# Performance work log

Hardware: AMD Instinct MI355X
Metric: run time of the kernel (lower is better)

The kernel has to match this reference:

```python
import jax, jax.numpy as jnp
import numpy as np
from jax.scipy.linalg import solve_triangular

B, S, HIDDEN = 2, 2048, 2048
HK, HV, DK, DV = 16, 32, 128, 128
KCONV = 4
CHUNK = 64
EPS = 1e-6
KEY_DIM = HK * DK        # 2048
VALUE_DIM = HV * DV      # 4096
CONV_DIM = 2 * KEY_DIM + VALUE_DIM  # 8192


def setup_inputs() -> dict:
    key = jax.random.key(0)
    ks = jax.random.split(key, 8)
    s = lambda n: 1.0 / np.sqrt(n)
    return {
        "hidden_states": jax.random.normal(ks[0], (B, S, HIDDEN), jnp.float32),
        "W_qkvz": jax.random.normal(ks[1], (HIDDEN, 2 * KEY_DIM + 2 * VALUE_DIM), jnp.float32) * s(HIDDEN),
        "W_ba": jax.random.normal(ks[2], (HIDDEN, 2 * HV), jnp.float32) * s(HIDDEN),
        "conv_weight": jax.random.normal(ks[3], (CONV_DIM, KCONV), jnp.float32) * s(KCONV),
        "dt_bias": jnp.ones((HV,), jnp.float32),
        "A_log": jax.random.normal(ks[4], (HV,), jnp.float32) * 0.1,
        "norm_weight": jnp.ones((DV,), jnp.float32),
        "W_out": jax.random.normal(ks[5], (VALUE_DIM, HIDDEN), jnp.float32) * s(VALUE_DIM),
    }


def _chunk_gated_delta_rule(q, k, v, g, beta):
    # q,k: [B,H,S,DK] (l2-normalized); v: [B,H,S,DV]; g,beta: [B,H,S]
    Bq, H, Sq, Dk = q.shape
    N = Sq // CHUNK
    q = q * (Dk ** -0.5)
    rs = lambda x: x.reshape(Bq, H, N, CHUNK, x.shape[-1])
    q, k, v = rs(q), rs(k), rs(v)
    g = g.reshape(Bq, H, N, CHUNK)
    beta = beta.reshape(Bq, H, N, CHUNK)
    gc = jnp.cumsum(g, axis=-1)  # within-chunk cumulative log-decay
    tri = jnp.tril(jnp.ones((CHUNK, CHUNK), bool))
    tri_s = jnp.tril(jnp.ones((CHUNK, CHUNK), bool), -1)
    decay = jnp.where(tri, jnp.exp(gc[..., :, None] - gc[..., None, :]), 0.0)
    k_beta = k * beta[..., None]
    v_beta = v * beta[..., None]
    # strictly-lower within-chunk interaction matrix; T = (I + A)^{-1} (fwd substitution)
    A = jnp.where(tri_s, jnp.einsum('bhncd,bhnkd->bhnck', k_beta, k) * decay, 0.0)
    eye = jnp.eye(CHUNK, dtype=q.dtype)
    T = solve_triangular(eye + A, jnp.broadcast_to(eye, A.shape), lower=True)
    v_adj = T @ v_beta                                    # [B,H,N,C,DV]
    k_cumdecay = T @ (k_beta * jnp.exp(gc)[..., None])    # [B,H,N,C,DK]
    attn_local = jnp.where(tri, jnp.einsum('bhncd,bhnkd->bhnck', q, k) * decay, 0.0)

    def step(state, xs):
        q_i, k_i, vadj_i, kcd_i, g_i, attn_i = xs          # per-chunk slices [B,H,C,*]
        v_new = vadj_i - kcd_i @ state                     # [B,H,C,DV]
        o = (q_i * jnp.exp(g_i)[..., None]) @ state + attn_i @ v_new
        g_last = g_i[..., -1]                              # [B,H]
        decayed_k = k_i * jnp.exp(g_last[..., None] - g_i)[..., None]
        state = state * jnp.exp(g_last)[..., None, None] + jnp.einsum('bhcd,bhcv->bhdv', decayed_k, v_new)
        return state, o

    mv = lambda x: jnp.moveaxis(x, 2, 0)
    state0 = jnp.zeros((Bq, H, Dk, v.shape[-1]), q.dtype)
    _, o = jax.lax.scan(step, state0, (mv(q), mv(k), mv(v_adj), mv(k_cumdecay), mv(gc), mv(attn_local)))
    return jnp.moveaxis(o, 0, 2).reshape(Bq, H, Sq, -1)


def reference(hidden_states, W_qkvz, W_ba, conv_weight, dt_bias, A_log, norm_weight, W_out):
    B_, S_, _ = hidden_states.shape
    # fused QKVZ / BA projections, contiguous layout [q|k|v|z], [b|a]
    qkvz = hidden_states @ W_qkvz
    q, k, v, z = jnp.split(qkvz, [KEY_DIM, 2 * KEY_DIM, 2 * KEY_DIM + VALUE_DIM], axis=-1)
    b, a = jnp.split(hidden_states @ W_ba, 2, axis=-1)
    beta = jax.nn.sigmoid(b)                                   # [B,S,HV]
    g = -jnp.exp(A_log) * jax.nn.softplus(a + dt_bias)         # [B,S,HV]
    # causal depthwise conv over [q|k|v] channels + silu
    mixed = jnp.concatenate([q, k, v], axis=-1)                # [B,S,CONV_DIM]
    pad = jnp.pad(mixed, ((0, 0), (KCONV - 1, 0), (0, 0)))
    conv = sum(pad[:, j:j + S_, :] * conv_weight[:, j] for j in range(KCONV))
    conv = jax.nn.silu(conv)
    q, k, v = jnp.split(conv, [KEY_DIM, 2 * KEY_DIM], axis=-1)
    q = q.reshape(B_, S_, HK, DK)
    k = k.reshape(B_, S_, HK, DK)
    v = v.reshape(B_, S_, HV, DV)
    l2n = lambda x: x * jax.lax.rsqrt(jnp.sum(x * x, -1, keepdims=True) + 1e-6)
    q, k = l2n(q), l2n(k)
    rep = HV // HK  # each qk head serves rep consecutive v heads
    q = jnp.repeat(q, rep, axis=2)
    k = jnp.repeat(k, rep, axis=2)
    tr = lambda x: jnp.swapaxes(x, 1, 2)                       # -> [B,H,S,D]
    o = _chunk_gated_delta_rule(tr(q), tr(k), tr(v), jnp.swapaxes(g, 1, 2), jnp.swapaxes(beta, 1, 2))
    o = jnp.swapaxes(o, 1, 2)                                  # [B,S,HV,DV]
    # gated RMSNorm (norm before gate): rmsnorm(o) * w * silu(z)
    z = z.reshape(B_, S_, HV, DV)
    o = o * jax.lax.rsqrt(jnp.mean(o * o, -1, keepdims=True) + EPS)
    o = o * norm_weight * jax.nn.silu(z)
    return o.reshape(B_, S_, VALUE_DIM) @ W_out
```

## Files before the change

### kernel.cpp

```cpp
#include <hip/hip_runtime.h>
#include <hip/hip_bf16.h>


typedef short bf16x8 __attribute__((ext_vector_type(8)));
typedef float f32x4  __attribute__((ext_vector_type(4)));

#define MFMA_BF16(a,b,c) __builtin_amdgcn_mfma_f32_16x16x32_bf16((a),(b),(c),0,0,0)
#define GLD16(g,l) __builtin_amdgcn_global_load_lds((const __attribute__((address_space(1))) void*)(g), (__attribute__((address_space(3))) void*)(l), 16, 0, 0)

__device__ __forceinline__ unsigned short f2bf(float x){
  union { float f; unsigned u; } v; v.f = x;
  return (unsigned short)((v.u + 0x7fffu + ((v.u >> 16) & 1u)) >> 16);
}
__device__ __forceinline__ float bf2f(unsigned short h){
  union { unsigned u; float f; } v; v.u = ((unsigned)h) << 16; return v.f;
}
__device__ __forceinline__ unsigned long long pack4bf(float a, float b, float c, float d){
  return (unsigned long long)f2bf(a) | ((unsigned long long)f2bf(b) << 16)
       | ((unsigned long long)f2bf(c) << 32) | ((unsigned long long)f2bf(d) << 48);
}

__global__ __launch_bounds__(256) void cast_bf16_kernel(
    const float* __restrict__ in, unsigned short* __restrict__ out, int n)
{
  int i = (blockIdx.x * 256 + threadIdx.x) * 4;
  if (i >= n) return;
  float4 v = *(const float4*)(in + i);
  *(unsigned long long*)(out + i) = pack4bf(v.x, v.y, v.z, v.w);
}

__global__ __launch_bounds__(256) void transpose_cast_kernel(
    const float* __restrict__ W, unsigned short* __restrict__ WT, int R, int C)
{
  __shared__ __attribute__((aligned(16))) float tile[32][33];
  int c0 = blockIdx.x * 32, r0 = blockIdx.y * 32;
  int tx = threadIdx.x & 31, ty = threadIdx.x >> 5;
  #pragma unroll
  for (int i = 0; i < 32; i += 8)
    tile[ty + i][tx] = W[(size_t)(r0 + ty + i) * C + c0 + tx];
  __syncthreads();
  #pragma unroll
  for (int i = 0; i < 32; i += 8)
    WT[(size_t)(c0 + ty + i) * R + r0 + tx] = f2bf(tile[tx][ty + i]);
}

__global__ __launch_bounds__(512, 2) void gemm256_bt(
    const unsigned short* __restrict__ A,
    const unsigned short* __restrict__ B,
    unsigned short* __restrict__ C, int M, int N, int K)
{
  __shared__ __attribute__((aligned(16))) unsigned short lds[65536];

  const int tid  = threadIdx.x;
  const int wave = tid >> 6, lane = tid & 63;
  const int quad = lane >> 4, l16 = lane & 15;
  const int wm8 = (wave >> 2) << 3;
  const int wn4 = (wave & 3) << 2;

  int wg = blockIdx.x;
  if ((gridDim.x & 7) == 0) {
    int qq = (int)gridDim.x >> 3;
    wg = (wg & 7) * qq + (wg >> 3);
  }
  const int tm = M >> 8;
  const int m0 = (wg % tm) << 8;
  const int n0 = (wg / tm) << 8;

  const int rd_off = ((l16 << 6) + (quad << 4)) ^ ((l16 >> 3) << 5);

  const int st_off = wave << 9;
  const int src_c  = ((wave & 1) << 5) + (((lane & 3) << 3) ^ ((lane >> 5) << 4));
  const unsigned short* Asrc = A + (size_t)(m0 + ((wave >> 1) << 4) + (lane >> 2)) * K + src_c;
  const unsigned short* Bsrc = B + (size_t)(n0 + ((wave >> 1) << 4) + (lane >> 2)) * K + src_c;

  const int NT = K >> 6;

#define STA(t, qi) GLD16(Asrc + (size_t)(qi) * 64 * K + (t) * 64, \
                         lds + (((t) & 1) << 15) + st_off + ((qi) << 12))
#define STB(t, qi) GLD16(Bsrc + (size_t)(qi) * 64 * K + (t) * 64, \
                         lds + (((t) & 1) << 15) + 16384 + st_off + ((qi) << 12))
#define RDA(dst, P)                                                            \
  _Pragma("unroll")                                                            \
  for (int j = 0; j < 2; ++j)                                                  \
    _Pragma("unroll")                                                          \
    for (int kb = 0; kb < 2; ++kb)                                             \
      dst[j][kb] = *(const bf16x8*)(Ar + ((((wm8 + 2 * (P) + j) << 1) | kb) << 10) + rd_off);
#define MMA(P, AF)                                                             \
  __builtin_amdgcn_s_setprio(1);                                               \
  _Pragma("unroll")                                                            \
  for (int j = 0; j < 2; ++j)                                                  \
    _Pragma("unroll")                                                          \
    for (int nf = 0; nf < 4; ++nf)                                             \
      _Pragma("unroll")                                                        \
      for (int kb = 0; kb < 2; ++kb)                                           \
        acc[2 * (P) + j][nf] = MFMA_BF16(AF[j][kb], b8[nf][kb], acc[2 * (P) + j][nf]); \
  __builtin_amdgcn_s_setprio(0);
#define LGKM4  asm volatile("s_waitcnt lgkmcnt(4)" ::: "memory");              \
               __builtin_amdgcn_sched_barrier(0)
#define LGKM0  asm volatile("s_waitcnt lgkmcnt(0)" ::: "memory");              \
               __builtin_amdgcn_sched_barrier(0)

  f32x4 acc[8][4];
  #pragma unroll
  for (int a = 0; a < 8; ++a)
    #pragma unroll
    for (int b = 0; b < 4; ++b)
      #pragma unroll
      for (int r = 0; r < 4; ++r) acc[a][b][r] = 0.f;

  STB(0, 0); STB(0, 1); STB(0, 2); STB(0, 3);
  STA(0, 0); STA(0, 1); STA(0, 2); STA(0, 3);
  if (NT > 1) {
    STB(1, 0); STB(1, 1); STB(1, 2); STB(1, 3); STA(1, 0); STA(1, 2);
    asm volatile("s_waitcnt vmcnt(6)" ::: "memory");
  } else {
    asm volatile("s_waitcnt vmcnt(0)" ::: "memory");
  }
  __builtin_amdgcn_s_barrier();

  for (int u = 0; u < NT; ++u) {
    const char* Ar = (const char*)lds + ((u & 1) << 16);
    const char* Br = Ar + 32768;
    bf16x8 b8[4][2], aA[2][2], aB[2][2];
    #pragma unroll
    for (int nf = 0; nf < 4; ++nf)
      #pragma unroll
      for (int kb = 0; kb < 2; ++kb)
        b8[nf][kb] = *(const bf16x8*)(Br + ((((wn4 + nf) << 1) | kb) << 10) + rd_off);
    RDA(aA, 0);
    __builtin_amdgcn_sched_barrier(0);

    RDA(aB, 1);
    if (u + 1 < NT) { STA(u + 1, 1); STA(u + 1, 3); }
    __builtin_amdgcn_s_barrier();
    LGKM4;
    MMA(0, aA);
    __builtin_amdgcn_s_barrier();

    RDA(aA, 2);
    if (u + 2 < NT) { STB(u + 2, 0); STB(u + 2, 1); }
    __builtin_amdgcn_s_barrier();
    LGKM4;
    MMA(1, aB);
    __builtin_amdgcn_s_barrier();

    RDA(aB, 3);
    if (u + 2 < NT) { STB(u + 2, 2); STA(u + 2, 0); }
    __builtin_amdgcn_s_barrier();
    LGKM4;
    MMA(2, aA);
    __builtin_amdgcn_s_barrier();

    if (u + 2 < NT) { STB(u + 2, 3); STA(u + 2, 2); }
    __builtin_amdgcn_s_barrier();
    LGKM0;
    MMA(3, aB);
    if (u + 2 < NT) asm volatile("s_waitcnt vmcnt(6)" ::: "memory");
    else            asm volatile("s_waitcnt vmcnt(0)" ::: "memory");
    __builtin_amdgcn_s_barrier();
  }
#undef RDA
#undef MMA
#undef LGKM4
#undef LGKM0
#undef STA
#undef STB

  #pragma unroll
  for (int mt = 0; mt < 8; ++mt) {
    int row = m0 + ((wave >> 2) << 7) + mt * 16 + (quad << 2);
    #pragma unroll
    for (int nf = 0; nf < 4; ++nf) {
      int col = n0 + ((wave & 3) << 6) + nf * 16 + l16;
      #pragma unroll
      for (int r = 0; r < 4; ++r)
        C[(size_t)(row + r) * N + col] = f2bf(acc[mt][nf][r]);
    }
  }
}

__global__ __launch_bounds__(512, 2) void gemm128x256_bt(
    const unsigned short* __restrict__ A,
    const unsigned short* __restrict__ B,
    float* __restrict__ C, int M, int N, int K)
{
  __shared__ __attribute__((aligned(16))) unsigned short lds[49152];

  const int tid  = threadIdx.x;
  const int wave = tid >> 6, lane = tid & 63;
  const int quad = lane >> 4, l16 = lane & 15;
  const int wm4 = (wave >> 2) << 2;
  const int wn4 = (wave & 3) << 2;

  int wg = blockIdx.x;
  if ((gridDim.x & 7) == 0) {
    int qq = (int)gridDim.x >> 3;
    wg = (wg & 7) * qq + (wg >> 3);
  }
  const int tm = M >> 7;
  const int m0 = (wg % tm) << 7;
  const int n0 = (wg / tm) << 8;

  const int rd_off = ((l16 << 6) + (quad << 4)) ^ ((l16 >> 3) << 5);
  const int st_off = wave << 9;
  const int src_c  = ((wave & 1) << 5) + (((lane & 3) << 3) ^ ((lane >> 5) << 4));
  const unsigned short* Asrc = A + (size_t)(m0 + ((wave >> 1) << 4) + (lane >> 2)) * K + src_c;
  const unsigned short* Bsrc = B + (size_t)(n0 + ((wave >> 1) << 4) + (lane >> 2)) * K + src_c;

  const int NT = K >> 6;

#define STA(t, qi) GLD16(Asrc + (size_t)(qi) * 64 * K + (t) * 64, \
                         lds + (((t) & 1) * 24576) + st_off + ((qi) << 12))
#define STB(t, qi) GLD16(Bsrc + (size_t)(qi) * 64 * K + (t) * 64, \
                         lds + (((t) & 1) * 24576) + 8192 + st_off + ((qi) << 12))

  f32x4 acc[4][4];
  #pragma unroll
  for (int a = 0; a < 4; ++a)
    #pragma unroll
    for (int b = 0; b < 4; ++b)
      #pragma unroll
      for (int r = 0; r < 4; ++r) acc[a][b][r] = 0.f;

  STB(0, 0); STB(0, 1); STB(0, 2); STB(0, 3);
  STA(0, 0); STA(0, 1);
  if (NT > 1) {
    STB(1, 0); STB(1, 1); STB(1, 2); STB(1, 3);
    asm volatile("s_waitcnt vmcnt(4)" ::: "memory");
  } else {
    asm volatile("s_waitcnt vmcnt(0)" ::: "memory");
  }
  __builtin_amdgcn_s_barrier();

  for (int u = 0; u < NT; ++u) {
    const char* Ar = (const char*)lds + (u & 1) * 49152;
    const char* Br = Ar + 16384;
    bf16x8 b8[4][2], aA[2][2], aB[2][2];
    #pragma unroll
    for (int nf = 0; nf < 4; ++nf)
      #pragma unroll
      for (int kb = 0; kb < 2; ++kb)
        b8[nf][kb] = *(const bf16x8*)(Br + ((((wn4 + nf) << 1) | kb) << 10) + rd_off);
    #pragma unroll
    for (int j = 0; j < 2; ++j)
      #pragma unroll
      for (int kb = 0; kb < 2; ++kb)
        aA[j][kb] = *(const bf16x8*)(Ar + ((((wm4 + j) << 1) | kb) << 10) + rd_off);
    __builtin_amdgcn_sched_barrier(0);

    #pragma unroll
    for (int j = 0; j < 2; ++j)
      #pragma unroll
      for (int kb = 0; kb < 2; ++kb)
        aB[j][kb] = *(const bf16x8*)(Ar + ((((wm4 + 2 + j) << 1) | kb) << 10) + rd_off);
    if (u + 1 < NT) { STA(u + 1, 0); STA(u + 1, 1); }
    __builtin_amdgcn_s_barrier();
    asm volatile("s_waitcnt lgkmcnt(4)" ::: "memory");
    __builtin_amdgcn_sched_barrier(0);
    __builtin_amdgcn_s_setprio(1);
    #pragma unroll
    for (int j = 0; j < 2; ++j)
      #pragma unroll
      for (int nf = 0; nf < 4; ++nf)
        #pragma unroll
        for (int kb = 0; kb < 2; ++kb)
          acc[j][nf] = MFMA_BF16(aA[j][kb], b8[nf][kb], acc[j][nf]);
    __builtin_amdgcn_s_setprio(0);
    __builtin_amdgcn_s_barrier();

    if (u + 2 < NT) { STB(u + 2, 0); STB(u + 2, 1); STB(u + 2, 2); STB(u + 2, 3); }
    __builtin_amdgcn_s_barrier();
    asm volatile("s_waitcnt lgkmcnt(0)" ::: "memory");
    __builtin_amdgcn_sched_barrier(0);
    __builtin_amdgcn_s_setprio(1);
    #pragma unroll
    for (int j = 0; j < 2; ++j)
      #pragma unroll
      for (int nf = 0; nf < 4; ++nf)
        #pragma unroll
        for (int kb = 0; kb < 2; ++kb)
          acc[2 + j][nf] = MFMA_BF16(aB[j][kb], b8[nf][kb], acc[2 + j][nf]);
    __builtin_amdgcn_s_setprio(0);
    if (u + 2 < NT) asm volatile("s_waitcnt vmcnt(4)" ::: "memory");
    else            asm volatile("s_waitcnt vmcnt(0)" ::: "memory");
    __builtin_amdgcn_s_barrier();
  }
#undef STA
#undef STB

  #pragma unroll
  for (int mt = 0; mt < 4; ++mt) {
    int row = m0 + ((wave >> 2) << 6) + mt * 16 + (quad << 2);
    #pragma unroll
    for (int nf = 0; nf < 4; ++nf) {
      int col = n0 + ((wave & 3) << 6) + nf * 16 + l16;
      #pragma unroll
      for (int r = 0; r < 4; ++r)
        C[(size_t)(row + r) * N + col] = acc[mt][nf][r];
    }
  }
}

__global__ __launch_bounds__(256) void ba_kernel(
    const float* __restrict__ H, const float* __restrict__ Wba,
    const float* __restrict__ dtb, const float* __restrict__ Alog,
    float* __restrict__ bbuf, float* __restrict__ gbuf)
{
  int t = threadIdx.x;
  int col = t & 63, wv = t >> 6;
  int m0 = blockIdx.x * 16 + wv * 4;
  const float* h0 = H + (size_t)m0 * 2048;
  float a0 = 0.f, a1 = 0.f, a2 = 0.f, a3 = 0.f;
  for (int k = 0; k < 2048; ++k) {
    float w = Wba[k * 64 + col];
    a0 += h0[k]        * w;
    a1 += h0[2048 + k] * w;
    a2 += h0[4096 + k] * w;
    a3 += h0[6144 + k] * w;
  }
  float accv[4] = {a0, a1, a2, a3};
  #pragma unroll
  for (int r = 0; r < 4; ++r) {
    int m = m0 + r;
    int b = m >> 11, s = m & 2047;
    float acc = accv[r];
    if (col < 32) {
      bbuf[((size_t)(b * 32 + col)) * 2048 + s] = 1.f / (1.f + __expf(-acc));
    } else {
      int hh = col - 32;
      float x  = acc + dtb[hh];
      float sp = (x > 20.f) ? x : log1pf(__expf(x));
      gbuf[((size_t)(b * 32 + hh)) * 2048 + s] = -__expf(Alog[hh]) * sp;
    }
  }
}

__global__ __launch_bounds__(128) void conv_kernel(
    const unsigned short* __restrict__ qkvz, const float* __restrict__ cw,
    unsigned short* __restrict__ qn, unsigned short* __restrict__ kn,
    unsigned short* __restrict__ vb)
{
  int s_base = blockIdx.x * 4;
  int head   = blockIdx.y * 8 + (threadIdx.x >> 4);
  int c8     = (threadIdx.x & 15) * 8;
  int col    = head * 128 + c8;
  int s_loc  = s_base & 2047;

  float vin[7][8];
  #pragma unroll
  for (int t = 0; t < 7; ++t) {
    int sp = s_loc + t - 3;
    if (sp >= 0) {
      bf16x8 v = *(const bf16x8*)(qkvz + (size_t)(s_base + t - 3) * 12288 + col);
      #pragma unroll
      for (int j = 0; j < 8; ++j) vin[t][j] = bf2f((unsigned short)v[j]);
    } else {
      #pragma unroll
      for (int j = 0; j < 8; ++j) vin[t][j] = 0.f;
    }
  }
  float w[8][4];
  #pragma unroll
  for (int j = 0; j < 8; ++j) {
    float4 wv = *(const float4*)(cw + (size_t)(col + j) * 4);
    w[j][0] = wv.x; w[j][1] = wv.y; w[j][2] = wv.z; w[j][3] = wv.w;
  }
  float y[4][8];
  #pragma unroll
  for (int u = 0; u < 4; ++u)
    #pragma unroll
    for (int j = 0; j < 8; ++j) {
      float acc = vin[u][j]*w[j][0] + vin[u+1][j]*w[j][1]
                + vin[u+2][j]*w[j][2] + vin[u+3][j]*w[j][3];
      y[u][j] = acc / (1.f + __expf(-acc));
    }

  if (head < 32) {
    #pragma unroll
    for (int u = 0; u < 4; ++u) {
      float ss = 0.f;
      #pragma unroll
      for (int j = 0; j < 8; ++j) ss += y[u][j] * y[u][j];
      ss += __shfl_xor(ss, 1);
      ss += __shfl_xor(ss, 2);
      ss += __shfl_xor(ss, 4);
      ss += __shfl_xor(ss, 8);
      float r = rsqrtf(ss + 1e-6f);
      bf16x8 out;
      if (head < 16) {
        float rq = r * 0.08838834764831845f;
        #pragma unroll
        for (int j = 0; j < 8; ++j) out[j] = (short)f2bf(y[u][j] * rq);
        *(bf16x8*)(qn + ((size_t)(s_base + u) * 16 + head) * 128 + c8) = out;
      } else {
        #pragma unroll
        for (int j = 0; j < 8; ++j) out[j] = (short)f2bf(y[u][j] * r);
        *(bf16x8*)(kn + ((size_t)(s_base + u) * 16 + (head - 16)) * 128 + c8) = out;
      }
    }
  } else {
    #pragma unroll
    for (int u = 0; u < 4; ++u) {
      bf16x8 out;
      #pragma unroll
      for (int j = 0; j < 8; ++j) out[j] = (short)f2bf(y[u][j]);
      *(bf16x8*)(vb + ((size_t)(s_base + u) * 32 + (head - 32)) * 128 + c8) = out;
    }
  }
}

__global__ __launch_bounds__(256) void chunk_kernel(
    const unsigned short* __restrict__ qnb, const unsigned short* __restrict__ knb,
    const unsigned short* __restrict__ vbb,
    const float* __restrict__ gbuf, const float* __restrict__ bbuf,
    unsigned short* __restrict__ attnb, unsigned short* __restrict__ vadjb,
    unsigned short* __restrict__ kcdn, unsigned short* __restrict__ qgb,
    unsigned short* __restrict__ kdT, float* __restrict__ egl)
{
  int cid = blockIdx.x;
  int n = cid & 31, h = (cid >> 5) & 31, b = cid >> 10;
  int h2 = h >> 1, s0 = n * 64;
  int gs0 = b * 2048 + s0;
  int tid = threadIdx.x, wave = tid >> 6, lane = tid & 63, quad = lane >> 4, l16 = lane & 15;

  __shared__ __attribute__((aligned(16))) unsigned short kS[64 * 136];
  __shared__ __attribute__((aligned(16))) float As[64 * 68];
  __shared__ float gcS[64], betaS[64];
  __shared__ float rsV[64], rsK[64], egq[64], egliS[64];

  if (tid < 64) {
    gcS[tid]   = gbuf[((size_t)(b * 32 + h)) * 2048 + s0 + tid];
    betaS[tid] = bbuf[((size_t)(b * 32 + h)) * 2048 + s0 + tid];
  }
  {
    int i = tid >> 2, seg = tid & 3;
    const bf16x8* kp = (const bf16x8*)(knb + ((size_t)(gs0 + i) * 16 + h2) * 128 + seg * 32);
    bf16x8* kd_ = (bf16x8*)(kS + i * 136 + seg * 32);
    #pragma unroll
    for (int u = 0; u < 4; ++u) kd_[u] = kp[u];
  }
  __syncthreads();
  if (tid == 0) {
    float run = 0.f;
    for (int i = 0; i < 64; ++i) { run += gcS[i]; gcS[i] = run; }
  }
  __syncthreads();

  if (tid < 64) {
    float gi = gcS[tid];
    rsV[tid]   = betaS[tid];
    rsK[tid]   = betaS[tid] * __expf(gi);
    egq[tid]   = __expf(gi);
    egliS[tid] = __expf(gcS[63] - gi);
    if (tid == 0) egl[cid] = __expf(gcS[63]);
  }

  {
    int arow = wave * 16 + l16;
    float bscale = betaS[arow];
    const unsigned short* qpg = qnb + ((size_t)(gs0 + arow) * 16 + h2) * 128;
    bf16x8 kbf[4], qf[4];
    #pragma unroll
    for (int ks = 0; ks < 4; ++ks) {
      bf16x8 kfr = *(const bf16x8*)(kS + arow * 136 + ks * 32 + quad * 8);
      bf16x8 t;
      #pragma unroll
      for (int e = 0; e < 8; ++e)
        t[e] = (short)f2bf(bf2f((unsigned short)kfr[e]) * bscale);
      kbf[ks] = t;
      qf[ks] = *(const bf16x8*)(qpg + ks * 32 + quad * 8);
    }
    #pragma unroll
    for (int jt = 0; jt < 4; ++jt) {
      f32x4 accA, accQ;
      #pragma unroll
      for (int r = 0; r < 4; ++r) { accA[r] = 0.f; accQ[r] = 0.f; }
      #pragma unroll
      for (int ks = 0; ks < 4; ++ks) {
        bf16x8 bfr = *(const bf16x8*)(kS + (jt * 16 + l16) * 136 + ks * 32 + quad * 8);
        accA = MFMA_BF16(kbf[ks], bfr, accA);
        accQ = MFMA_BF16(qf[ks],  bfr, accQ);
      }
      #pragma unroll
      for (int r = 0; r < 4; ++r) {
        int i = wave * 16 + quad * 4 + r;
        int j = jt * 16 + l16;
        float e = __expf(gcS[i] - gcS[j]);
        As[i * 68 + j] = (j < i) ? (accA[r] * e) : 0.f;
        attnb[(size_t)cid * 4096 + i * 64 + j] = (j <= i) ? f2bf(accQ[r] * e) : (unsigned short)0;
      }
    }
  }
  __syncthreads();

  {
    int c = tid;
    float x[64];
    if (c < 128) {
      const unsigned short* vp = vbb + ((size_t)gs0 * 32 + h) * 128 + c;
      #pragma unroll
      for (int i = 0; i < 64; ++i)
        x[i] = bf2f(vp[(size_t)i * 4096]) * rsV[i];
    } else {
      int ck = c - 128;
      #pragma unroll
      for (int i = 0; i < 64; ++i)
        x[i] = bf2f(kS[i * 136 + ck]) * rsK[i];
    }
    #pragma unroll
    for (int bi = 0; bi < 4; ++bi) {
      const int base = bi * 16;
      #pragma unroll
      for (int ii = 1; ii < 16; ++ii) {
        const int r = base + ii;
        const f32x4* ar = (const f32x4*)(As + r * 68 + base);
        float s = 0.f;
        #pragma unroll
        for (int g = 0; g < 4; ++g) {
          f32x4 a4 = ar[g];
          s += a4[0] * x[base + g*4] + a4[1] * x[base + g*4 + 1]
             + a4[2] * x[base + g*4 + 2] + a4[3] * x[base + g*4 + 3];
        }
        x[r] -= s;
      }
      #pragma unroll
      for (int r = base + 16; r < 64; ++r) {
        const f32x4* ar = (const f32x4*)(As + r * 68 + base);
        float s = 0.f;
        #pragma unroll
        for (int g = 0; g < 4; ++g) {
          f32x4 a4 = ar[g];
          s += a4[0] * x[base + g*4] + a4[1] * x[base + g*4 + 1]
             + a4[2] * x[base + g*4 + 2] + a4[3] * x[base + g*4 + 3];
        }
        x[r] -= s;
      }
    }
    if (c < 128) {
      unsigned short* vo = vadjb + (size_t)cid * 8192 + c;
      #pragma unroll
      for (int i = 0; i < 64; ++i) vo[i * 128] = f2bf(x[i]);
    } else {
      unsigned short* ko = kcdn + (size_t)cid * 8192 + (c - 128);
      #pragma unroll
      for (int i = 0; i < 64; ++i) ko[i * 128] = f2bf(-x[i]);
    }
  }

  {
    int i = tid >> 2, seg = tid & 3;
    float egli = egliS[i];
    float eqi  = egq[i];
    size_t base128 = (size_t)cid * 8192 + i * 128 + seg * 32;
    const unsigned short* qp = qnb + ((size_t)(gs0 + i) * 16 + h2) * 128 + seg * 32;
    #pragma unroll
    for (int u = 0; u < 32; u += 4) {
      *(unsigned long long*)(qgb + base128 + u) =
          pack4bf(bf2f(qp[u]) * eqi, bf2f(qp[u+1]) * eqi, bf2f(qp[u+2]) * eqi, bf2f(qp[u+3]) * eqi);
    }
    const unsigned short* kp = kS + i * 136 + seg * 32;
    unsigned short* kdo = kdT + (size_t)cid * 8192;
    #pragma unroll
    for (int u = 0; u < 32; ++u) {
      int d = seg * 32 + u;
      kdo[(size_t)d * 64 + i] = f2bf(bf2f(kp[u]) * egli);
    }
  }
}

struct ScanPref {
  bf16x8 kf[4], qf[4], af2[2], kdf[2][2];
  float  vinit[2][4];
  float  a;
};

__device__ __forceinline__ void scan_load(
    ScanPref& p, size_t cid,
    const unsigned short* __restrict__ qgb, const unsigned short* __restrict__ kcdn,
    const unsigned short* __restrict__ attnb, const unsigned short* __restrict__ kdT,
    const unsigned short* __restrict__ vadjb, const float* __restrict__ egl,
    int w, int quad, int l16, int dv0)
{
  const unsigned short* qgc = qgb  + cid * 8192;
  const unsigned short* kcc = kcdn + cid * 8192;
  const unsigned short* atc = attnb + cid * 4096;
  const unsigned short* kdc = kdT  + cid * 8192;
  const unsigned short* vac = vadjb + cid * 8192;
  p.a = egl[cid];
  #pragma unroll
  for (int ks = 0; ks < 4; ++ks) {
    p.kf[ks] = *(const bf16x8*)(kcc + (size_t)(w * 16 + l16) * 128 + ks * 32 + quad * 8);
    p.qf[ks] = *(const bf16x8*)(qgc + (size_t)(w * 16 + l16) * 128 + ks * 32 + quad * 8);
  }
  #pragma unroll
  for (int k2 = 0; k2 < 2; ++k2)
    p.af2[k2] = *(const bf16x8*)(atc + (size_t)(w * 16 + l16) * 64 + k2 * 32 + quad * 8);
  #pragma unroll
  for (int mi = 0; mi < 2; ++mi)
    #pragma unroll
    for (int k2 = 0; k2 < 2; ++k2)
      p.kdf[mi][k2] = *(const bf16x8*)(kdc + (size_t)((w * 2 + mi) * 16 + l16) * 64 + k2 * 32 + quad * 8);
  #pragma unroll
  for (int ni = 0; ni < 2; ++ni)
    #pragma unroll
    for (int r = 0; r < 4; ++r)
      p.vinit[ni][r] = bf2f(vac[(size_t)(w * 16 + quad * 4 + r) * 128 + dv0 + ni * 16 + l16]);
}

__device__ __forceinline__ void scan_step(
    const ScanPref& p, f32x4 st[2][2],
    unsigned short* stT, unsigned short* vnT,
    unsigned short* __restrict__ obuf, int bh, int n,
    int w, int quad, int l16, int dv0)
{
  bf16x8 sf[2][4];
  #pragma unroll
  for (int ni = 0; ni < 2; ++ni)
    #pragma unroll
    for (int ks = 0; ks < 4; ++ks)
      sf[ni][ks] = *(const bf16x8*)(stT + (ni * 16 + l16) * 136 + ks * 32 + quad * 8);

  f32x4 vacc[2];
  #pragma unroll
  for (int ni = 0; ni < 2; ++ni)
    #pragma unroll
    for (int r = 0; r < 4; ++r) vacc[ni][r] = p.vinit[ni][r];
  #pragma unroll
  for (int ni = 0; ni < 2; ++ni)
    #pragma unroll
    for (int ks = 0; ks < 4; ++ks)
      vacc[ni] = MFMA_BF16(p.kf[ks], sf[ni][ks], vacc[ni]);

  f32x4 oacc[2];
  #pragma unroll
  for (int ni = 0; ni < 2; ++ni)
    #pragma unroll
    for (int r = 0; r < 4; ++r) oacc[ni][r] = 0.f;
  #pragma unroll
  for (int ni = 0; ni < 2; ++ni)
    #pragma unroll
    for (int ks = 0; ks < 4; ++ks)
      oacc[ni] = MFMA_BF16(p.qf[ks], sf[ni][ks], oacc[ni]);

  #pragma unroll
  for (int ni = 0; ni < 2; ++ni)
    #pragma unroll
    for (int r = 0; r < 4; ++r)
      vnT[(ni * 16 + l16) * 72 + w * 16 + quad * 4 + r] = f2bf(vacc[ni][r]);
  __syncthreads();

  bf16x8 vf[2][2];
  #pragma unroll
  for (int ni = 0; ni < 2; ++ni)
    #pragma unroll
    for (int k2 = 0; k2 < 2; ++k2)
      vf[ni][k2] = *(const bf16x8*)(vnT + (ni * 16 + l16) * 72 + k2 * 32 + quad * 8);
  #pragma unroll
  for (int ni = 0; ni < 2; ++ni)
    #pragma unroll
    for (int k2 = 0; k2 < 2; ++k2)
      oacc[ni] = MFMA_BF16(p.af2[k2], vf[ni][k2], oacc[ni]);
  unsigned short* op = obuf + ((size_t)bh * 2048 + n * 64) * 128;
  #pragma unroll
  for (int ni = 0; ni < 2; ++ni)
    #pragma unroll
    for (int r = 0; r < 4; ++r)
      op[(size_t)(w * 16 + quad * 4 + r) * 128 + dv0 + ni * 16 + l16] = f2bf(oacc[ni][r]);

  #pragma unroll
  for (int mi = 0; mi < 2; ++mi) {
    #pragma unroll
    for (int ni = 0; ni < 2; ++ni) {
      f32x4 acc_;
      #pragma unroll
      for (int r = 0; r < 4; ++r) acc_[r] = p.a * st[mi][ni][r];
      #pragma unroll
      for (int k2 = 0; k2 < 2; ++k2)
        acc_ = MFMA_BF16(p.kdf[mi][k2], vf[ni][k2], acc_);
      st[mi][ni] = acc_;
    }
  }
  #pragma unroll
  for (int mi = 0; mi < 2; ++mi)
    #pragma unroll
    for (int ni = 0; ni < 2; ++ni)
      #pragma unroll
      for (int r = 0; r < 4; ++r)
        stT[(ni * 16 + l16) * 136 + (w * 2 + mi) * 16 + quad * 4 + r] = f2bf(st[mi][ni][r]);
  __syncthreads();
}

__global__ __launch_bounds__(256, 1) void scan_kernel(
    const unsigned short* __restrict__ qgb, const unsigned short* __restrict__ kcdn,
    const unsigned short* __restrict__ attnb, const unsigned short* __restrict__ kdT,
    const unsigned short* __restrict__ vadjb, const float* __restrict__ egl,
    unsigned short* __restrict__ obuf)
{
  int bh = blockIdx.x, dv0 = blockIdx.y * 32;
  int tid = threadIdx.x, w = tid >> 6, quad = (tid & 63) >> 4, l16 = tid & 15;
  __shared__ __attribute__((aligned(16))) unsigned short stT[32 * 136];
  __shared__ __attribute__((aligned(16))) unsigned short vnT[32 * 72];

  for (int idx = tid; idx < 32 * 136; idx += 256) stT[idx] = 0;
  f32x4 st[2][2];
  #pragma unroll
  for (int a = 0; a < 2; ++a)
    #pragma unroll
    for (int bq = 0; bq < 2; ++bq)
      #pragma unroll
      for (int r = 0; r < 4; ++r) st[a][bq][r] = 0.f;

  ScanPref pA, pB;
  scan_load(pA, (size_t)bh * 32, qgb, kcdn, attnb, kdT, vadjb, egl, w, quad, l16, dv0);
  __syncthreads();

  for (int n = 0; n < 32; n += 2) {
    scan_load(pB, (size_t)bh * 32 + n + 1, qgb, kcdn, attnb, kdT, vadjb, egl, w, quad, l16, dv0);
    scan_step(pA, st, stT, vnT, obuf, bh, n, w, quad, l16, dv0);
    if (n + 2 < 32)
      scan_load(pA, (size_t)bh * 32 + n + 2, qgb, kcdn, attnb, kdT, vadjb, egl, w, quad, l16, dv0);
    scan_step(pB, st, stT, vnT, obuf, bh, n + 1, w, quad, l16, dv0);
  }
}

__global__ __launch_bounds__(256) void gate_kernel(
    const unsigned short* __restrict__ obuf, const unsigned short* __restrict__ qkvz,
    const float* __restrict__ nw, unsigned short* __restrict__ gated)
{
  int id = blockIdx.x * 16 + (threadIdx.x >> 4);
  int h = id & 31, bs = id >> 5;
  int b = bs >> 11, s = bs & 2047;
  int c8 = (threadIdx.x & 15) * 8;
  const unsigned short* op = obuf + (((size_t)(b * 32 + h)) * 2048 + s) * 128 + c8;
  const unsigned short* zp = qkvz + (size_t)bs * 12288 + 8192 + h * 128 + c8;

  bf16x8 xv = *(const bf16x8*)op;
  float x[8];
  float ss = 0.f;
  #pragma unroll
  for (int j = 0; j < 8; ++j) { x[j] = bf2f((unsigned short)xv[j]); ss += x[j] * x[j]; }
  ss += __shfl_xor(ss, 1);
  ss += __shfl_xor(ss, 2);
  ss += __shfl_xor(ss, 4);
  ss += __shfl_xor(ss, 8);
  float r = rsqrtf(ss * (1.f / 128.f) + 1e-6f);

  bf16x8 zv = *(const bf16x8*)zp;
  float4 nw0 = *(const float4*)(nw + c8);
  float4 nw1 = *(const float4*)(nw + c8 + 4);
  float nwv[8] = {nw0.x, nw0.y, nw0.z, nw0.w, nw1.x, nw1.y, nw1.z, nw1.w};
  bf16x8 out;
  #pragma unroll
  for (int j = 0; j < 8; ++j) {
    float z = bf2f((unsigned short)zv[j]);
    float g = z / (1.f + __expf(-z));
    out[j] = (short)f2bf(x[j] * r * nwv[j] * g);
  }
  *(bf16x8*)(gated + (size_t)bs * 4096 + h * 128 + c8) = out;
}

extern "C" void kernel_launch(void* const* d_in, const int* in_sizes, int n_in,
                              void* d_out, int out_size, void* d_ws, size_t ws_size,
                              hipStream_t stream)
{
  const float* H     = (const float*)d_in[0];
  const float* Wqkvz = (const float*)d_in[1];
  const float* Wba   = (const float*)d_in[2];
  const float* cw    = (const float*)d_in[3];
  const float* dtb   = (const float*)d_in[4];
  const float* Alog  = (const float*)d_in[5];
  const float* nw    = (const float*)d_in[6];
  const float* Wout  = (const float*)d_in[7];
  float* out = (float*)d_out;

  const size_t U1 = 0;
  const size_t U2 = U1 + 67108864;
  const size_t U3 = U2 + 100663296;
  const size_t U4 = U3 + 16777216;
  const size_t U5 = U4 + 1048576;
  const size_t U6 = U5 + 151003136;
  const size_t NEED = U6 + 33554432;
  if (ws_size < NEED) return;

  char* base = (char*)d_ws;
  unsigned short* Hbf   = (unsigned short*)(base + U1);
  unsigned short* WqT   = (unsigned short*)(base + U1 + 16777216);
  unsigned short* qnb   = (unsigned short*)(base + U1);
  unsigned short* knb   = (unsigned short*)(base + U1 + 16777216);
  unsigned short* vbb   = (unsigned short*)(base + U1 + 33554432);
  unsigned short* qkvzb = (unsigned short*)(base + U2);
  unsigned short* WoT   = (unsigned short*)(base + U3);
  float*          bbuf  = (float*)(base + U4);
  float*          gbuf  = (float*)(base + U4 + 524288);
  unsigned short* attnb = (unsigned short*)(base + U5);
  unsigned short* vadjb = (unsigned short*)(base + U5 + 16777216);
  unsigned short* kcdn  = (unsigned short*)(base + U5 + 50331648);
  unsigned short* qgb   = (unsigned short*)(base + U5 + 83886080);
  unsigned short* kdTb  = (unsigned short*)(base + U5 + 117440512);
  float*          egl   = (float*)(base + U5 + 150994944);
  unsigned short* gated = (unsigned short*)(base + U5);
  unsigned short* obuf  = (unsigned short*)(base + U6);

  cast_bf16_kernel<<<8192, 256, 0, stream>>>(H, Hbf, 4096 * 2048);
  transpose_cast_kernel<<<dim3(12288 / 32, 2048 / 32), 256, 0, stream>>>(Wqkvz, WqT, 2048, 12288);
  transpose_cast_kernel<<<dim3(2048 / 32, 4096 / 32), 256, 0, stream>>>(Wout, WoT, 4096, 2048);
  gemm256_bt<<<768, 512, 0, stream>>>(Hbf, WqT, qkvzb, 4096, 12288, 2048);
  ba_kernel<<<256, 256, 0, stream>>>(H, Wba, dtb, Alog, bbuf, gbuf);
  conv_kernel<<<dim3(1024, 8), 128, 0, stream>>>(qkvzb, cw, qnb, knb, vbb);
  chunk_kernel<<<2048, 256, 0, stream>>>(qnb, knb, vbb, gbuf, bbuf, attnb, vadjb, kcdn, qgb, kdTb, egl);
  scan_kernel<<<dim3(64, 4), 256, 0, stream>>>(qgb, kcdn, attnb, kdTb, vadjb, egl, obuf);
  gate_kernel<<<8192, 256, 0, stream>>>(obuf, qkvzb, nw, gated);
  gemm128x256_bt<<<256, 512, 0, stream>>>(gated, WoT, out, 4096, 2048, 4096);
}
```

Measured before the change: 852.3 us.

## Deepen scan prefetch to three stages, split ba rows, drop GEMM swizzle

The scan kernel now keeps three prefetch buffers in flight instead of two, hiding more global-load latency behind the serial chunk recurrence at the cost of more registers. The ba projection kernel now gives each wave a single row with float4 loads of the hidden state and launches four times as many blocks, for more parallelism. The XCD-aware block remapping in the main GEMM is removed, which may change L2 locality across chiplets.

```diff
diff --git a/kernel.cpp b/kernel.cpp
--- a/kernel.cpp
+++ b/kernel.cpp
@@ -57,11 +57,7 @@
   const int wm8 = (wave >> 2) << 3;
   const int wn4 = (wave & 3) << 2;
 
-  int wg = blockIdx.x;
-  if ((gridDim.x & 7) == 0) {
-    int qq = (int)gridDim.x >> 3;
-    wg = (wg & 7) * qq + (wg >> 3);
-  }
+  const int wg = blockIdx.x;
   const int tm = M >> 8;
   const int m0 = (wg % tm) << 8;
   const int n0 = (wg / tm) << 8;
@@ -308,30 +304,24 @@
 {
   int t = threadIdx.x;
   int col = t & 63, wv = t >> 6;
-  int m0 = blockIdx.x * 16 + wv * 4;
-  const float* h0 = H + (size_t)m0 * 2048;
-  float a0 = 0.f, a1 = 0.f, a2 = 0.f, a3 = 0.f;
-  for (int k = 0; k < 2048; ++k) {
-    float w = Wba[k * 64 + col];
-    a0 += h0[k]        * w;
-    a1 += h0[2048 + k] * w;
-    a2 += h0[4096 + k] * w;
-    a3 += h0[6144 + k] * w;
-  }
-  float accv[4] = {a0, a1, a2, a3};
-  #pragma unroll
-  for (int r = 0; r < 4; ++r) {
-    int m = m0 + r;
-    int b = m >> 11, s = m & 2047;
-    float acc = accv[r];
-    if (col < 32) {
-      bbuf[((size_t)(b * 32 + col)) * 2048 + s] = 1.f / (1.f + __expf(-acc));
-    } else {
-      int hh = col - 32;
-      float x  = acc + dtb[hh];
-      float sp = (x > 20.f) ? x : log1pf(__expf(x));
-      gbuf[((size_t)(b * 32 + hh)) * 2048 + s] = -__expf(Alog[hh]) * sp;
-    }
+  int m = blockIdx.x * 4 + wv;
+  const float* h0 = H + (size_t)m * 2048;
+  float acc = 0.f;
+  for (int k = 0; k < 2048; k += 4) {
+    float4 hv = *(const float4*)(h0 + k);
+    acc += hv.x * Wba[(k + 0) * 64 + col];
+    acc += hv.y * Wba[(k + 1) * 64 + col];
+    acc += hv.z * Wba[(k + 2) * 64 + col];
+    acc += hv.w * Wba[(k + 3) * 64 + col];
+  }
+  int b = m >> 11, s = m & 2047;
+  if (col < 32) {
+    bbuf[((size_t)(b * 32 + col)) * 2048 + s] = 1.f / (1.f + __expf(-acc));
+  } else {
+    int hh = col - 32;
+    float x  = acc + dtb[hh];
+    float sp = (x > 20.f) ? x : log1pf(__expf(x));
+    gbuf[((size_t)(b * 32 + hh)) * 2048 + s] = -__expf(Alog[hh]) * sp;
   }
 }
 
@@ -710,16 +700,27 @@
       #pragma unroll
       for (int r = 0; r < 4; ++r) st[a][bq][r] = 0.f;
 
-  ScanPref pA, pB;
-  scan_load(pA, (size_t)bh * 32, qgb, kcdn, attnb, kdT, vadjb, egl, w, quad, l16, dv0);
+  size_t base = (size_t)bh * 32;
+  ScanPref pA, pB, pC;
+  scan_load(pA, base + 0, qgb, kcdn, attnb, kdT, vadjb, egl, w, quad, l16, dv0);
+  scan_load(pB, base + 1, qgb, kcdn, attnb, kdT, vadjb, egl, w, quad, l16, dv0);
+  scan_load(pC, base + 2, qgb, kcdn, attnb, kdT, vadjb, egl, w, quad, l16, dv0);
   __syncthreads();
 
-  for (int n = 0; n < 32; n += 2) {
-    scan_load(pB, (size_t)bh * 32 + n + 1, qgb, kcdn, attnb, kdT, vadjb, egl, w, quad, l16, dv0);
+  for (int n = 0; n < 32; n += 3) {
     scan_step(pA, st, stT, vnT, obuf, bh, n, w, quad, l16, dv0);
-    if (n + 2 < 32)
-      scan_load(pA, (size_t)bh * 32 + n + 2, qgb, kcdn, attnb, kdT, vadjb, egl, w, quad, l16, dv0);
-    scan_step(pB, st, stT, vnT, obuf, bh, n + 1, w, quad, l16, dv0);
+    if (n + 3 < 32)
+      scan_load(pA, base + n + 3, qgb, kcdn, attnb, kdT, vadjb, egl, w, quad, l16, dv0);
+    if (n + 1 < 32) {
+      scan_step(pB, st, stT, vnT, obuf, bh, n + 1, w, quad, l16, dv0);
+      if (n + 4 < 32)
+        scan_load(pB, base + n + 4, qgb, kcdn, attnb, kdT, vadjb, egl, w, quad, l16, dv0);
+    }
+    if (n + 2 < 32) {
+      scan_step(pC, st, stT, vnT, obuf, bh, n + 2, w, quad, l16, dv0);
+      if (n + 5 < 32)
+        scan_load(pC, base + n + 5, qgb, kcdn, attnb, kdT, vadjb, egl, w, quad, l16, dv0);
+    }
   }
 }
 
@@ -805,7 +806,7 @@
   transpose_cast_kernel<<<dim3(12288 / 32, 2048 / 32), 256, 0, stream>>>(Wqkvz, WqT, 2048, 12288);
   transpose_cast_kernel<<<dim3(2048 / 32, 4096 / 32), 256, 0, stream>>>(Wout, WoT, 4096, 2048);
   gemm256_bt<<<768, 512, 0, stream>>>(Hbf, WqT, qkvzb, 4096, 12288, 2048);
-  ba_kernel<<<256, 256, 0, stream>>>(H, Wba, dtb, Alog, bbuf, gbuf);
+  ba_kernel<<<1024, 256, 0, stream>>>(H, Wba, dtb, Alog, bbuf, gbuf);
   conv_kernel<<<dim3(1024, 8), 128, 0, stream>>>(qkvzb, cw, qnb, knb, vbb);
   chunk_kernel<<<2048, 256, 0, stream>>>(qnb, knb, vbb, gbuf, bbuf, attnb, vadjb, kcdn, qgb, kdTb, egl);
   scan_kernel<<<dim3(64, 4), 256, 0, stream>>>(qgb, kcdn, attnb, kdTb, vadjb, egl, obuf);
```

New measurement: 870.1 us. 1.02x slower.
